# Performance work log

Measured on AMD Instinct MI355X. Metric: run time of the kernel, lower is better.

The kernel has to match this reference:

```python
import jax, jax.numpy as jnp
import numpy as np

B, C, H, W = 16, 16, 256, 256
HID, OUT_C, IN_C = 128, 13, 3

_SOBEL_X = np.array([[-1, 0, 1], [-2, 0, 2], [-1, 0, 1]], dtype=np.float32)
_SOBEL_Y = _SOBEL_X.T


def setup_inputs() -> dict:
    key = jax.random.key(0)
    k1, k2, k3, k4 = jax.random.split(key, 4)
    return {
        "input_grid": jax.random.normal(k1, (B, C, H, W), dtype=jnp.float32),
        "w1": jax.random.normal(k2, (HID, 3 * C), dtype=jnp.float32) * 0.0001,
        "b1": jax.random.normal(k3, (HID,), dtype=jnp.float32) * 0.0001,
        "w2": jax.random.normal(k4, (OUT_C, HID), dtype=jnp.float32) * 0.0001,
    }


def _depthwise_sobel(x_padded, filt2d):
    # x_padded: [B, C, H+2, W+2]; depthwise 3x3 valid conv (groups=C)
    c = x_padded.shape[1]
    kern = jnp.broadcast_to(jnp.asarray(filt2d)[None, None], (c, 1, 3, 3))
    return jax.lax.conv_general_dilated(
        x_padded, kern, window_strides=(1, 1), padding="VALID",
        feature_group_count=c,
        dimension_numbers=("NCHW", "OIHW", "NCHW"))


def reference(input_grid, w1, b1, w2):
    # circular pad by 1 on spatial dims
    xp = jnp.pad(input_grid, ((0, 0), (0, 0), (1, 1), (1, 1)), mode="wrap")
    gx = _depthwise_sobel(xp, _SOBEL_X)
    gy = _depthwise_sobel(xp, _SOBEL_Y)
    # perception grid: [B, 3C, H, W]
    perception = jnp.concatenate([input_grid, gx, gy], axis=1)
    # update network: 1x1 conv -> ReLU -> 1x1 conv (dropout = identity in eval)
    h = jax.nn.relu(jnp.einsum("bchw,oc->bohw", perception, w1)
                    + b1[None, :, None, None])
    ds = jnp.einsum("bchw,oc->bohw", h, w2)  # [B, C-IN_C, H, W]
    # residual add to channels 3: of the state
    return input_grid.at[:, IN_C:].add(ds)
```

## Files before the change

### kernel.cpp

```cpp
#include <hip/hip_runtime.h>

#define BB   16
#define CC   16
#define HH   256
#define WW   256
#define HID  128
#define OUTC 13

typedef short short8 __attribute__((ext_vector_type(8)));
typedef float floatx16 __attribute__((ext_vector_type(16)));

__device__ __forceinline__ unsigned short f2bf(float x) {
    unsigned int u = __float_as_uint(x);
    u += 0x7fffu + ((u >> 16) & 1u);
    return (unsigned short)(u >> 16);
}

#define W1F_BYTES 36864
#define W2F_OFF   36864

__global__ __launch_bounds__(256) void gca_prep(
    const float* __restrict__ w1, const float* __restrict__ w2,
    unsigned char* __restrict__ ws)
{
    const int id = blockIdx.x * 256 + threadIdx.x;
    const float SX[9] = {-1.f, 0.f, 1.f, -2.f, 0.f, 2.f, -1.f, 0.f, 1.f};
    const float SY[9] = {-1.f, -2.f, -1.f, 0.f, 0.f, 0.f, 1.f, 2.f, 1.f};

    if (id < 2304) {
        const int mtG  = id / 576;
        const int rem  = id % 576;
        const int tap  = rem / 64;
        const int lane = rem % 64;
        const int p  = lane & 31, hi = lane >> 5;
        const int hid = 32 * mtG + p;
        const float cen = (tap == 4) ? 1.f : 0.f;
        const float sxv = SX[tap], syv = SY[tap];
        const float* wr = w1 + hid * 48;
        unsigned int o[4];
        for (int k = 0; k < 4; ++k) {
            int c0 = 8 * hi + 2 * k;
            float v0 = wr[c0]     * cen + wr[16 + c0]     * sxv + wr[32 + c0]     * syv;
            float v1 = wr[c0 + 1] * cen + wr[16 + c0 + 1] * sxv + wr[32 + c0 + 1] * syv;
            o[k] = (unsigned int)f2bf(v0) | ((unsigned int)f2bf(v1) << 16);
        }
        *(uint4*)(ws + (size_t)id * 16) = make_uint4(o[0], o[1], o[2], o[3]);
    } else if (id < 2816) {
        const int id2 = id - 2304;
        const int s    = id2 / 64;
        const int lane = id2 % 64;
        const int outc = lane & 31, hi = lane >> 5;
        unsigned int o[4];
        for (int k = 0; k < 4; ++k) {
            int hid0 = 16 * s + 8 * hi + 2 * k;
            float v0 = (outc < OUTC) ? w2[outc * HID + hid0]     : 0.f;
            float v1 = (outc < OUTC) ? w2[outc * HID + hid0 + 1] : 0.f;
            o[k] = (unsigned int)f2bf(v0) | ((unsigned int)f2bf(v1) << 16);
        }
        *(uint4*)(ws + W2F_OFF + (size_t)id2 * 16) = make_uint4(o[0], o[1], o[2], o[3]);
    }
}

#define TILE_DW 6120
#define CBUF_DW 2304

__global__ __launch_bounds__(256) void gca_main(
    const float* __restrict__ in,
    const float* __restrict__ b1,
    const unsigned char* __restrict__ ws,
    float* __restrict__ out)
{
    __shared__ unsigned int lds[TILE_DW + CBUF_DW];

    const int tid  = threadIdx.x;
    const int wid  = tid >> 6;
    const int lane = tid & 63;
    const int hw   = wid & 1;
    const int P    = wid >> 1;
    const int p    = lane & 31;
    const int hi   = lane >> 5;

    const int bI = blockIdx.x >> 7;
    const int rm = blockIdx.x & 127;
    const int y0 = (rm >> 3) << 4;
    const int x0 = (rm & 7)  << 5;

    {
        unsigned short* tus = (unsigned short*)lds;
        const float* inb = in + ((size_t)bI << 20);
        for (int i = tid; i < 16 * 18 * 34; i += 256) {
            int c   = i / 612;
            int rem = i % 612;
            int row = rem / 34;
            int col = rem % 34;
            int y = (y0 + row - 1) & 255;
            int x = (x0 + col - 1) & 255;
            float v = inb[(c << 16) + (y << 8) + x];
            tus[(row * 34 + col) * 20 + c] = f2bf(v);
        }
    }
    __syncthreads();

    const unsigned char* w1f = ws + ((size_t)(2 * hw) * 9) * 64 * 16;
    const unsigned char* w2f = ws + W2F_OFF + (size_t)(4 * hw) * 64 * 16;
    const int cb = TILE_DW + P * (64 * 18) + lane * 18;

#pragma unroll 1
    for (int t = 0; t < 8; ++t) {
        const int row = y0 + 2 * t + P;

        floatx16 acc1[2];
#pragma unroll
        for (int m = 0; m < 2; ++m) {
            const int hb = 64 * hw + 32 * m + 4 * hi;
#pragma unroll
            for (int rr = 0; rr < 4; ++rr) {
                float4 bv = *(const float4*)(b1 + hb + 8 * rr);
                acc1[m][4 * rr + 0] = bv.x;
                acc1[m][4 * rr + 1] = bv.y;
                acc1[m][4 * rr + 2] = bv.z;
                acc1[m][4 * rr + 3] = bv.w;
            }
        }

#pragma unroll
        for (int tap = 0; tap < 9; ++tap) {
            const int tr  = 2 * t + P + tap / 3;
            const int col = p + tap % 3;
            const int dwo = (tr * 34 + col) * 10 + 4 * hi;
            union { unsigned int u[4]; short8 s; } bfr;
            uint2 lo2 = *(const uint2*)&lds[dwo];
            uint2 hi2 = *(const uint2*)&lds[dwo + 2];
            bfr.u[0] = lo2.x; bfr.u[1] = lo2.y; bfr.u[2] = hi2.x; bfr.u[3] = hi2.y;
#pragma unroll
            for (int m = 0; m < 2; ++m) {
                short8 af = *(const short8*)(w1f + (size_t)((m * 9 + tap) * 64 + lane) * 16);
                acc1[m] = __builtin_amdgcn_mfma_f32_32x32x16_bf16(af, bfr.s, acc1[m], 0, 0, 0);
            }
        }

        uint2 hrun[8];
#pragma unroll
        for (int m = 0; m < 2; ++m)
#pragma unroll
            for (int rr = 0; rr < 4; ++rr) {
                float h0 = fmaxf(acc1[m][4 * rr + 0], 0.f);
                float h1 = fmaxf(acc1[m][4 * rr + 1], 0.f);
                float h2 = fmaxf(acc1[m][4 * rr + 2], 0.f);
                float h3 = fmaxf(acc1[m][4 * rr + 3], 0.f);
                hrun[4 * m + rr].x = (unsigned int)f2bf(h0) | ((unsigned int)f2bf(h1) << 16);
                hrun[4 * m + rr].y = (unsigned int)f2bf(h2) | ((unsigned int)f2bf(h3) << 16);
            }

        floatx16 acc2 = {};
#pragma unroll
        for (int sp = 0; sp < 4; ++sp) {
            uint2 r0 = hrun[2 * sp];
            uint2 r1 = hrun[2 * sp + 1];
            uint2 x0s, x1s;
            x0s.x = (unsigned int)__shfl_xor((int)r0.x, 32);
            x0s.y = (unsigned int)__shfl_xor((int)r0.y, 32);
            x1s.x = (unsigned int)__shfl_xor((int)r1.x, 32);
            x1s.y = (unsigned int)__shfl_xor((int)r1.y, 32);
            union { unsigned int u[4]; short8 s; } b2;
            uint2 lo = hi ? x1s : r0;
            uint2 hg = hi ? r1  : x0s;
            b2.u[0] = lo.x; b2.u[1] = lo.y; b2.u[2] = hg.x; b2.u[3] = hg.y;
            short8 a2 = *(const short8*)(w2f + (size_t)(sp * 64 + lane) * 16);
            acc2 = __builtin_amdgcn_mfma_f32_32x32x16_bf16(a2, b2.s, acc2, 0, 0, 0);
        }

        if (hw == 1) {
#pragma unroll
            for (int k = 0; k < 8; ++k) {
                uint2 v;
                v.x = __float_as_uint(acc2[2 * k]);
                v.y = __float_as_uint(acc2[2 * k + 1]);
                *(uint2*)&lds[cb + 2 * k] = v;
            }
        }
        __syncthreads();

        if (hw == 0) {
#pragma unroll
            for (int r = 0; r < 16; ++r) {
                int outc = (r & 3) + 8 * (r >> 2) + 4 * hi;
                if (outc < OUTC) {
                    float sum = acc2[r] + __uint_as_float(lds[cb + r]);
                    int idx = ((bI * 16 + 3 + outc) << 16) + (row << 8) + x0 + p;
                    out[idx] = in[idx] + sum;
                }
            }
        } else {
#pragma unroll
            for (int k = 0; k < 2; ++k) {
                int e = lane + 64 * k;
                if (e < 96) {
                    int c  = e >> 5;
                    int px = e & 31;
                    int idx = ((bI * 16 + c) << 16) + (row << 8) + x0 + px;
                    out[idx] = in[idx];
                }
            }
        }
        __syncthreads();
    }
}

extern "C" void kernel_launch(void* const* d_in, const int* in_sizes, int n_in,
                              void* d_out, int out_size, void* d_ws, size_t ws_size,
                              hipStream_t stream) {
    const float* x  = (const float*)d_in[0];
    const float* w1 = (const float*)d_in[1];
    const float* b1 = (const float*)d_in[2];
    const float* w2 = (const float*)d_in[3];
    float* out = (float*)d_out;
    unsigned char* ws = (unsigned char*)d_ws;

    hipLaunchKernelGGL(gca_prep, dim3(11), dim3(256), 0, stream, w1, w2, ws);
    hipLaunchKernelGGL(gca_main, dim3(2048), dim3(256), 0, stream, x, b1, ws, out);
}
```

Measured before the change: 214.2 us.

## Restructure tile load, pass-through copy and epilogue with split reduction exchange

Rewrites the tile staging so each thread loads a channel pair per row and packs it with the hardware bf16 pack instruction, replacing scattered per-element loads. The first three channels are copied with vectorized nontemporal stores once per block instead of per row. The residual input is preloaded into the second-stage accumulator and w2 fragments are hoisted out of the row loop. The cross-wave partial-sum exchange is split so both wave halves write and read half the outputs through double-buffered LDS, which removes the trailing barrier. Occupancy is hinted with a launch bound of 4 blocks per CU. Switching to hardware bf16 conversion may change rounding behaviour slightly.

Measured after the change: 342.5 us. 1.6x slower.

```diff
diff --git a/kernel.cpp b/kernel.cpp
--- a/kernel.cpp
+++ b/kernel.cpp
@@ -9,11 +9,18 @@
 
 typedef short short8 __attribute__((ext_vector_type(8)));
 typedef float floatx16 __attribute__((ext_vector_type(16)));
+typedef float floatx4 __attribute__((ext_vector_type(4)));
 
 __device__ __forceinline__ unsigned short f2bf(float x) {
     unsigned int u = __float_as_uint(x);
     u += 0x7fffu + ((u >> 16) & 1u);
     return (unsigned short)(u >> 16);
+}
+
+__device__ __forceinline__ unsigned int cvt_pk_bf16(float lo, float hi) {
+    unsigned int d;
+    asm("v_cvt_pk_bf16_f32 %0, %1, %2" : "=v"(d) : "v"(lo), "v"(hi));
+    return d;
 }
 
 #define W1F_BYTES 36864
@@ -62,15 +69,16 @@
 }
 
 #define TILE_DW 6120
-#define CBUF_DW 2304
-
-__global__ __launch_bounds__(256) void gca_main(
+#define CB_DW   1024
+#define LDS_DW  (TILE_DW + 2 * CB_DW)
+
+__global__ __launch_bounds__(256, 4) void gca_main(
     const float* __restrict__ in,
     const float* __restrict__ b1,
     const unsigned char* __restrict__ ws,
     float* __restrict__ out)
 {
-    __shared__ unsigned int lds[TILE_DW + CBUF_DW];
+    __shared__ unsigned int lds[LDS_DW];
 
     const int tid  = threadIdx.x;
     const int wid  = tid >> 6;
@@ -85,29 +93,72 @@
     const int y0 = (rm >> 3) << 4;
     const int x0 = (rm & 7)  << 5;
 
+    const float* inb  = in  + ((size_t)bI << 20);
+    float*       outb = out + ((size_t)bI << 20);
+
     {
-        unsigned short* tus = (unsigned short*)lds;
-        const float* inb = in + ((size_t)bI << 20);
-        for (int i = tid; i < 16 * 18 * 34; i += 256) {
-            int c   = i / 612;
-            int rem = i % 612;
-            int row = rem / 34;
-            int col = rem % 34;
-            int y = (y0 + row - 1) & 255;
-            int x = (x0 + col - 1) & 255;
-            float v = inb[(c << 16) + (y << 8) + x];
-            tus[(row * 34 + col) * 20 + c] = f2bf(v);
+        int e = tid;
+#pragma unroll
+        for (int it = 0; it < 2; ++it) {
+            if (e < 384) {
+                int c = e >> 7, rem = e & 127, rw = rem >> 3, q = rem & 7;
+                int idx = (c << 16) + ((y0 + rw) << 8) + x0 + (q << 2);
+                floatx4 v = *(const floatx4*)(inb + idx);
+                __builtin_nontemporal_store(v, (floatx4*)(outb + idx));
+            }
+            e += 256;
+        }
+    }
+
+    {
+        const int g = tid >> 5, l = tid & 31;
+        const float* cp = inb + ((size_t)(2 * g) << 16);
+        const int xA = (x0 + l - 1) & 255;
+        const int xB = (x0 + l + 31) & 255;
+        const int ldsA = l * 10 + g;
+        const int ldsB = (l + 32) * 10 + g;
+        const bool doB = (l < 2);
+        for (int rw = 0; rw < 18; ++rw) {
+            const int yo = ((y0 + rw - 1) & 255) << 8;
+            float a0 = cp[yo + xA], a1 = cp[yo + xA + 65536];
+            lds[rw * 340 + ldsA] = cvt_pk_bf16(a0, a1);
+            if (doB) {
+                float c0 = cp[yo + xB], c1 = cp[yo + xB + 65536];
+                lds[rw * 340 + ldsB] = cvt_pk_bf16(c0, c1);
+            }
         }
     }
     __syncthreads();
 
-    const unsigned char* w1f = ws + ((size_t)(2 * hw) * 9) * 64 * 16;
-    const unsigned char* w2f = ws + W2F_OFF + (size_t)(4 * hw) * 64 * 16;
-    const int cb = TILE_DW + P * (64 * 18) + lane * 18;
+    const unsigned char* w1f  = ws + ((size_t)(2 * hw) * 9) * 64 * 16;
+    const unsigned char* w2fp = ws + W2F_OFF + (size_t)(4 * hw) * 64 * 16;
+
+    short8 a2f[4];
+#pragma unroll
+    for (int sp = 0; sp < 4; ++sp)
+        a2f[sp] = *(const short8*)(w2fp + (size_t)(sp * 64 + lane) * 16);
+
+    int off_[4]; bool val_[4];
+#pragma unroll
+    for (int j = 0; j < 4; ++j) {
+        int r  = 2 * j + hw;
+        int oc = (r & 3) + 8 * (r >> 2) + 4 * hi;
+        val_[j] = (oc < OUTC);
+        off_[j] = (3 + oc) << 16;
+    }
+
+    const int mysec = TILE_DW + (P * 2 + hw)       * 256 + 2 * lane;
+    const int pasec = TILE_DW + (P * 2 + (1 - hw)) * 256 + 2 * lane;
 
 #pragma unroll 1
     for (int t = 0; t < 8; ++t) {
-        const int row = y0 + 2 * t + P;
+        const int row   = y0 + 2 * t + P;
+        const int ibase = (row << 8) + x0 + p;
+
+        float rs[4];
+#pragma unroll
+        for (int j = 0; j < 4; ++j)
+            rs[j] = val_[j] ? inb[ibase + off_[j]] : 0.f;
 
         floatx16 acc1[2];
 #pragma unroll
@@ -148,11 +199,14 @@
                 float h1 = fmaxf(acc1[m][4 * rr + 1], 0.f);
                 float h2 = fmaxf(acc1[m][4 * rr + 2], 0.f);
                 float h3 = fmaxf(acc1[m][4 * rr + 3], 0.f);
-                hrun[4 * m + rr].x = (unsigned int)f2bf(h0) | ((unsigned int)f2bf(h1) << 16);
-                hrun[4 * m + rr].y = (unsigned int)f2bf(h2) | ((unsigned int)f2bf(h3) << 16);
+                hrun[4 * m + rr].x = cvt_pk_bf16(h0, h1);
+                hrun[4 * m + rr].y = cvt_pk_bf16(h2, h3);
             }
 
         floatx16 acc2 = {};
+        if (hw == 0) { acc2[0] = rs[0]; acc2[2] = rs[1]; acc2[4] = rs[2]; acc2[6] = rs[3]; }
+        else         { acc2[1] = rs[0]; acc2[3] = rs[1]; acc2[5] = rs[2]; acc2[7] = rs[3]; }
+
 #pragma unroll
         for (int sp = 0; sp < 4; ++sp) {
             uint2 r0 = hrun[2 * sp];
@@ -166,44 +220,43 @@
             uint2 lo = hi ? x1s : r0;
             uint2 hg = hi ? r1  : x0s;
             b2.u[0] = lo.x; b2.u[1] = lo.y; b2.u[2] = hg.x; b2.u[3] = hg.y;
-            short8 a2 = *(const short8*)(w2f + (size_t)(sp * 64 + lane) * 16);
-            acc2 = __builtin_amdgcn_mfma_f32_32x32x16_bf16(a2, b2.s, acc2, 0, 0, 0);
-        }
-
-        if (hw == 1) {
-#pragma unroll
-            for (int k = 0; k < 8; ++k) {
-                uint2 v;
-                v.x = __float_as_uint(acc2[2 * k]);
-                v.y = __float_as_uint(acc2[2 * k + 1]);
-                *(uint2*)&lds[cb + 2 * k] = v;
-            }
-        }
+            acc2 = __builtin_amdgcn_mfma_f32_32x32x16_bf16(a2f[sp], b2.s, acc2, 0, 0, 0);
+        }
+
+        const int cb = mysec + (t & 1) * CB_DW;
+        uint2 wv0, wv1;
+        if (hw == 0) {
+            wv0.x = __float_as_uint(acc2[1]); wv0.y = __float_as_uint(acc2[3]);
+            wv1.x = __float_as_uint(acc2[5]); wv1.y = __float_as_uint(acc2[7]);
+        } else {
+            wv0.x = __float_as_uint(acc2[0]); wv0.y = __float_as_uint(acc2[2]);
+            wv1.x = __float_as_uint(acc2[4]); wv1.y = __float_as_uint(acc2[6]);
+        }
+        *(uint2*)&lds[cb]       = wv0;
+        *(uint2*)&lds[cb + 128] = wv1;
+
         __syncthreads();
 
+        const int pb = pasec + (t & 1) * CB_DW;
+        uint2 q0 = *(const uint2*)&lds[pb];
+        uint2 q1 = *(const uint2*)&lds[pb + 128];
+
+        float s_[4];
         if (hw == 0) {
-#pragma unroll
-            for (int r = 0; r < 16; ++r) {
-                int outc = (r & 3) + 8 * (r >> 2) + 4 * hi;
-                if (outc < OUTC) {
-                    float sum = acc2[r] + __uint_as_float(lds[cb + r]);
-                    int idx = ((bI * 16 + 3 + outc) << 16) + (row << 8) + x0 + p;
-                    out[idx] = in[idx] + sum;
-                }
-            }
+            s_[0] = acc2[0] + __uint_as_float(q0.x);
+            s_[1] = acc2[2] + __uint_as_float(q0.y);
+            s_[2] = acc2[4] + __uint_as_float(q1.x);
+            s_[3] = acc2[6] + __uint_as_float(q1.y);
         } else {
-#pragma unroll
-            for (int k = 0; k < 2; ++k) {
-                int e = lane + 64 * k;
-                if (e < 96) {
-                    int c  = e >> 5;
-                    int px = e & 31;
-                    int idx = ((bI * 16 + c) << 16) + (row << 8) + x0 + px;
-                    out[idx] = in[idx];
-                }
-            }
-        }
-        __syncthreads();
+            s_[0] = acc2[1] + __uint_as_float(q0.x);
+            s_[1] = acc2[3] + __uint_as_float(q0.y);
+            s_[2] = acc2[5] + __uint_as_float(q1.x);
+            s_[3] = acc2[7] + __uint_as_float(q1.y);
+        }
+#pragma unroll
+        for (int j = 0; j < 4; ++j)
+            if (val_[j])
+                __builtin_nontemporal_store(s_[j], &outb[ibase + off_[j]]);
     }
 }
 
```
